# Kernel tuning notes

Measured on AMD Instinct MI355X. Metric: run time of the kernel, lower is better.

## Reference

```python
import jax, jax.numpy as jnp
import numpy as np

ALPHA = 0.9  # EMAFusion temporal_fusion_alpha


def setup_inputs() -> dict:
    key = jax.random.key(0)
    y_seq = jax.random.normal(key, (4, 4096, 2048), dtype=jnp.float32)
    return {"y_seq": y_seq}


def reference(y_seq):
    # EMA recurrence: h_t = (1-alpha)*y_t + alpha*h_{t-1}, h_{-1}=0.
    # Original torch code detaches h_prev each step (backward-only effect),
    # mirrored here with stop_gradient on the carry.
    B, S, D = y_seq.shape
    h0 = jnp.zeros((B, D), dtype=y_seq.dtype)

    def step(h_prev, y_t):
        h_prev = jax.lax.stop_gradient(h_prev)
        h_t = (1.0 - ALPHA) * y_t + ALPHA * h_prev
        return h_t, h_t

    # scan over time axis: move S to leading dim
    _, out = jax.lax.scan(step, h0, jnp.swapaxes(y_seq, 0, 1))  # (S, B, D)
    return jnp.swapaxes(out, 0, 1)  # (B, S, D)
```

## Files before the change

kernel.cpp:

```cpp
#include <hip/hip_runtime.h>


typedef float v4 __attribute__((ext_vector_type(4)));

constexpr int B  = 4;
constexpr int S  = 4096;
constexpr int D  = 2048;
constexpr int D4 = D / 4;
constexpr int L  = 128;
constexpr int W  = 64;

__global__ __launch_bounds__(256, 1) void ema_kernel(const v4* __restrict__ y,
                                                     v4* __restrict__ out) {
    const int d4 = blockIdx.x * blockDim.x + threadIdx.x;
    const int c  = blockIdx.y;
    const int b  = blockIdx.z;

    const long long base = (long long)b * S * D4 + d4;
    const int sm = c * L;

    v4 h = (v4)(0.0f);
    const v4* __restrict__ p;

    v4 b0, b1, b2, b3, b4, b5, b6, b7;

#define LOAD_ALL() do {            \
        b0 = p[0 * D4];            \
        b1 = p[1 * D4];            \
        b2 = p[2 * D4];            \
        b3 = p[3 * D4];            \
        b4 = p[4 * D4];            \
        b5 = p[5 * D4];            \
        b6 = p[6 * D4];            \
        b7 = p[7 * D4];            \
        p += 8 * D4;               \
    } while (0)

#define EMA(bi) h = 0.9f * h + 0.1f * (bi)

    if (c != 0) {
        p = y + base + (long long)(sm - W) * D4;
        LOAD_ALL();
        #pragma unroll 1
        for (int g = 0; g < W / 8 - 1; ++g) {
            EMA(b0); b0 = p[0 * D4];
            EMA(b1); b1 = p[1 * D4];
            EMA(b2); b2 = p[2 * D4];
            EMA(b3); b3 = p[3 * D4];
            EMA(b4); b4 = p[4 * D4];
            EMA(b5); b5 = p[5 * D4];
            EMA(b6); b6 = p[6 * D4];
            EMA(b7); b7 = p[7 * D4];
            p += 8 * D4;
        }
        EMA(b0); EMA(b1); EMA(b2); EMA(b3);
        EMA(b4); EMA(b5); EMA(b6); EMA(b7);
    } else {
        p = y + base;
    }

    v4* __restrict__ q = out + base + (long long)sm * D4;
    LOAD_ALL();

#define STEP(i, bi)                                         \
        EMA(bi);                                            \
        __builtin_nontemporal_store(h, q + (i) * D4);       \
        bi = p[(i) * D4]

    #pragma unroll 1
    for (int g = 0; g < L / 8 - 1; ++g) {
        STEP(0, b0);
        STEP(1, b1);
        STEP(2, b2);
        STEP(3, b3);
        STEP(4, b4);
        STEP(5, b5);
        STEP(6, b6);
        STEP(7, b7);
        p += 8 * D4;
        q += 8 * D4;
    }
    EMA(b0); __builtin_nontemporal_store(h, q + 0 * D4);
    EMA(b1); __builtin_nontemporal_store(h, q + 1 * D4);
    EMA(b2); __builtin_nontemporal_store(h, q + 2 * D4);
    EMA(b3); __builtin_nontemporal_store(h, q + 3 * D4);
    EMA(b4); __builtin_nontemporal_store(h, q + 4 * D4);
    EMA(b5); __builtin_nontemporal_store(h, q + 5 * D4);
    EMA(b6); __builtin_nontemporal_store(h, q + 6 * D4);
    EMA(b7); __builtin_nontemporal_store(h, q + 7 * D4);

#undef STEP
#undef EMA
#undef LOAD_ALL
}

extern "C" void kernel_launch(void* const* d_in, const int* in_sizes, int n_in,
                              void* d_out, int out_size, void* d_ws, size_t ws_size,
                              hipStream_t stream) {
    const v4* y = (const v4*)d_in[0];
    v4* out = (v4*)d_out;

    dim3 block(256, 1, 1);
    dim3 grid(D4 / 256, S / L, B);
    ema_kernel<<<grid, block, 0, stream>>>(y, out);
}
```

Baseline: 237.0 us.

## Shorten time chunks and raise occupancy with double-buffered EMA loads

Cuts the per-block time chunk from 128 to 32 steps and raises the launch bound to 4 blocks per CU, so four times as many blocks run and more loads are in flight. The load path now uses two 8-deep register buffers (a/b) so one batch is in flight while the other is consumed. Early chunks get a warmup window shortened to the available history instead of a special case. The trade-off is extra traffic: each block still replays a 64-step warmup for only 32 outputs, which triples the input reads compared with 1.5x before, though most of those rereads may hit cache.

```diff
diff --git a/kernel.cpp b/kernel.cpp
--- a/kernel.cpp
+++ b/kernel.cpp
@@ -7,10 +7,10 @@
 constexpr int S  = 4096;
 constexpr int D  = 2048;
 constexpr int D4 = D / 4;
-constexpr int L  = 128;
+constexpr int L  = 32;
 constexpr int W  = 64;
 
-__global__ __launch_bounds__(256, 1) void ema_kernel(const v4* __restrict__ y,
+__global__ __launch_bounds__(256, 4) void ema_kernel(const v4* __restrict__ y,
                                                      v4* __restrict__ out) {
     const int d4 = blockIdx.x * blockDim.x + threadIdx.x;
     const int c  = blockIdx.y;
@@ -22,9 +22,22 @@
     v4 h = (v4)(0.0f);
     const v4* __restrict__ p;
 
+    v4 a0, a1, a2, a3, a4, a5, a6, a7;
     v4 b0, b1, b2, b3, b4, b5, b6, b7;
 
-#define LOAD_ALL() do {            \
+#define LOADA() do {               \
+        a0 = p[0 * D4];            \
+        a1 = p[1 * D4];            \
+        a2 = p[2 * D4];            \
+        a3 = p[3 * D4];            \
+        a4 = p[4 * D4];            \
+        a5 = p[5 * D4];            \
+        a6 = p[6 * D4];            \
+        a7 = p[7 * D4];            \
+        p += 8 * D4;               \
+    } while (0)
+
+#define LOADB() do {               \
         b0 = p[0 * D4];            \
         b1 = p[1 * D4];            \
         b2 = p[2 * D4];            \
@@ -36,62 +49,75 @@
         p += 8 * D4;               \
     } while (0)
 
-#define EMA(bi) h = 0.9f * h + 0.1f * (bi)
+#define EMA(x) (h = 0.9f * h + 0.1f * (x))
+#define EMAA() do { EMA(a0); EMA(a1); EMA(a2); EMA(a3); \
+                    EMA(a4); EMA(a5); EMA(a6); EMA(a7); } while (0)
+#define EMAB() do { EMA(b0); EMA(b1); EMA(b2); EMA(b3); \
+                    EMA(b4); EMA(b5); EMA(b6); EMA(b7); } while (0)
 
-    if (c != 0) {
-        p = y + base + (long long)(sm - W) * D4;
-        LOAD_ALL();
+    const int nw = (sm < W) ? sm : W;
+    p = y + base + (long long)(sm - nw) * D4;
+
+    if (nw) {
+        LOADA();
+        LOADB();
         #pragma unroll 1
-        for (int g = 0; g < W / 8 - 1; ++g) {
-            EMA(b0); b0 = p[0 * D4];
-            EMA(b1); b1 = p[1 * D4];
-            EMA(b2); b2 = p[2 * D4];
-            EMA(b3); b3 = p[3 * D4];
-            EMA(b4); b4 = p[4 * D4];
-            EMA(b5); b5 = p[5 * D4];
-            EMA(b6); b6 = p[6 * D4];
-            EMA(b7); b7 = p[7 * D4];
-            p += 8 * D4;
+        for (int g = 0; g < (nw / 8 - 2) / 2; ++g) {
+            EMAA(); LOADA();
+            EMAB(); LOADB();
         }
-        EMA(b0); EMA(b1); EMA(b2); EMA(b3);
-        EMA(b4); EMA(b5); EMA(b6); EMA(b7);
-    } else {
-        p = y + base;
+        EMAA();
+        EMAB();
     }
 
     v4* __restrict__ q = out + base + (long long)sm * D4;
-    LOAD_ALL();
 
-#define STEP(i, bi)                                         \
-        EMA(bi);                                            \
-        __builtin_nontemporal_store(h, q + (i) * D4);       \
-        bi = p[(i) * D4]
+    LOADA();
+    LOADB();
 
-    #pragma unroll 1
-    for (int g = 0; g < L / 8 - 1; ++g) {
-        STEP(0, b0);
-        STEP(1, b1);
-        STEP(2, b2);
-        STEP(3, b3);
-        STEP(4, b4);
-        STEP(5, b5);
-        STEP(6, b6);
-        STEP(7, b7);
-        p += 8 * D4;
-        q += 8 * D4;
-    }
-    EMA(b0); __builtin_nontemporal_store(h, q + 0 * D4);
-    EMA(b1); __builtin_nontemporal_store(h, q + 1 * D4);
-    EMA(b2); __builtin_nontemporal_store(h, q + 2 * D4);
-    EMA(b3); __builtin_nontemporal_store(h, q + 3 * D4);
-    EMA(b4); __builtin_nontemporal_store(h, q + 4 * D4);
-    EMA(b5); __builtin_nontemporal_store(h, q + 5 * D4);
-    EMA(b6); __builtin_nontemporal_store(h, q + 6 * D4);
-    EMA(b7); __builtin_nontemporal_store(h, q + 7 * D4);
+    EMA(a0); __builtin_nontemporal_store(h, q + 0 * D4);
+    EMA(a1); __builtin_nontemporal_store(h, q + 1 * D4);
+    EMA(a2); __builtin_nontemporal_store(h, q + 2 * D4);
+    EMA(a3); __builtin_nontemporal_store(h, q + 3 * D4);
+    EMA(a4); __builtin_nontemporal_store(h, q + 4 * D4);
+    EMA(a5); __builtin_nontemporal_store(h, q + 5 * D4);
+    EMA(a6); __builtin_nontemporal_store(h, q + 6 * D4);
+    EMA(a7); __builtin_nontemporal_store(h, q + 7 * D4);
+    LOADA();
 
-#undef STEP
+    EMA(b0); __builtin_nontemporal_store(h, q +  8 * D4);
+    EMA(b1); __builtin_nontemporal_store(h, q +  9 * D4);
+    EMA(b2); __builtin_nontemporal_store(h, q + 10 * D4);
+    EMA(b3); __builtin_nontemporal_store(h, q + 11 * D4);
+    EMA(b4); __builtin_nontemporal_store(h, q + 12 * D4);
+    EMA(b5); __builtin_nontemporal_store(h, q + 13 * D4);
+    EMA(b6); __builtin_nontemporal_store(h, q + 14 * D4);
+    EMA(b7); __builtin_nontemporal_store(h, q + 15 * D4);
+    LOADB();
+
+    EMA(a0); __builtin_nontemporal_store(h, q + 16 * D4);
+    EMA(a1); __builtin_nontemporal_store(h, q + 17 * D4);
+    EMA(a2); __builtin_nontemporal_store(h, q + 18 * D4);
+    EMA(a3); __builtin_nontemporal_store(h, q + 19 * D4);
+    EMA(a4); __builtin_nontemporal_store(h, q + 20 * D4);
+    EMA(a5); __builtin_nontemporal_store(h, q + 21 * D4);
+    EMA(a6); __builtin_nontemporal_store(h, q + 22 * D4);
+    EMA(a7); __builtin_nontemporal_store(h, q + 23 * D4);
+
+    EMA(b0); __builtin_nontemporal_store(h, q + 24 * D4);
+    EMA(b1); __builtin_nontemporal_store(h, q + 25 * D4);
+    EMA(b2); __builtin_nontemporal_store(h, q + 26 * D4);
+    EMA(b3); __builtin_nontemporal_store(h, q + 27 * D4);
+    EMA(b4); __builtin_nontemporal_store(h, q + 28 * D4);
+    EMA(b5); __builtin_nontemporal_store(h, q + 29 * D4);
+    EMA(b6); __builtin_nontemporal_store(h, q + 30 * D4);
+    EMA(b7); __builtin_nontemporal_store(h, q + 31 * D4);
+
+#undef EMAB
+#undef EMAA
 #undef EMA
-#undef LOAD_ALL
+#undef LOADB
+#undef LOADA
 }
 
 extern "C" void kernel_launch(void* const* d_in, const int* in_sizes, int n_in,
```

Result: slower. 255.2 us (+7.7%).

## Stage EMA input through LDS with async global_load_lds double buffering

Applied to the files above, without the earlier changes.

Global loads of y now go directly into shared memory through the global-to-LDS load builtin, using two 8-step buffers per wave. Explicit vmcnt waits and scheduling barriers replace the compiler-scheduled register prefetch. The aim is to keep more loads in flight and free VGPRs, so the serial EMA chain is fed with fewer stalls. In exchange it adds LDS round trips and hand-placed waits. Because stores also count toward vmcnt on CDNA, the waits may end up stricter than the loads alone need.

```diff
diff --git a/kernel.cpp b/kernel.cpp
--- a/kernel.cpp
+++ b/kernel.cpp
@@ -8,90 +8,93 @@
 constexpr int D  = 2048;
 constexpr int D4 = D / 4;
 constexpr int L  = 128;
-constexpr int W  = 64;
+
+#define SEAL() __builtin_amdgcn_sched_barrier(0)
+#define WAIT8() do { asm volatile("s_waitcnt vmcnt(8)" ::: "memory"); SEAL(); } while (0)
+#define WAIT0() do { asm volatile("s_waitcnt vmcnt(0)" ::: "memory"); SEAL(); } while (0)
 
 __global__ __launch_bounds__(256, 1) void ema_kernel(const v4* __restrict__ y,
                                                      v4* __restrict__ out) {
-    const int d4 = blockIdx.x * blockDim.x + threadIdx.x;
-    const int c  = blockIdx.y;
-    const int b  = blockIdx.z;
+    __shared__ v4 smem[4096];
+
+    const int tid  = threadIdx.x;
+    const int wave = tid >> 6;
+    const int lane = tid & 63;
+    const int d4   = blockIdx.x * blockDim.x + tid;
+    const int c    = blockIdx.y;
+    const int b    = blockIdx.z;
 
     const long long base = (long long)b * S * D4 + d4;
-    const int sm = c * L;
+    const int sm  = c * L;
+    const int nwg = (c == 0) ? 0 : 8;
+
+    const v4* p = y + base + (long long)(sm - 8 * nwg) * D4;
+    v4* q = out + base + (long long)sm * D4;
 
     v4 h = (v4)(0.0f);
-    const v4* __restrict__ p;
 
-    v4 b0, b1, b2, b3, b4, b5, b6, b7;
+#define SLOT(kb, s) ((((kb) * 8 + (s)) * 4 + wave) * 64)
 
-#define LOAD_ALL() do {            \
-        b0 = p[0 * D4];            \
-        b1 = p[1 * D4];            \
-        b2 = p[2 * D4];            \
-        b3 = p[3 * D4];            \
-        b4 = p[4 * D4];            \
-        b5 = p[5 * D4];            \
-        b6 = p[6 * D4];            \
-        b7 = p[7 * D4];            \
-        p += 8 * D4;               \
+#define ISSUE1(kb, s) \
+    __builtin_amdgcn_global_load_lds(p + (s) * D4, &smem[SLOT(kb, s)], 16, 0, 0)
+
+#define ISSUE(kb) do {                                      \
+        ISSUE1(kb, 0); ISSUE1(kb, 1); ISSUE1(kb, 2); ISSUE1(kb, 3); \
+        ISSUE1(kb, 4); ISSUE1(kb, 5); ISSUE1(kb, 6); ISSUE1(kb, 7); \
+        p += 8 * D4;                                        \
+        SEAL();                                             \
     } while (0)
 
-#define EMA(bi) h = 0.9f * h + 0.1f * (bi)
+#define EMA1(kb, s) do {                                    \
+        v4 x = smem[SLOT(kb, s) + lane];                    \
+        h = 0.9f * h + 0.1f * x;                            \
+    } while (0)
+
+#define CONS_NS(kb) do {                                    \
+        EMA1(kb, 0); EMA1(kb, 1); EMA1(kb, 2); EMA1(kb, 3); \
+        EMA1(kb, 4); EMA1(kb, 5); EMA1(kb, 6); EMA1(kb, 7); \
+        SEAL();                                             \
+    } while (0)
+
+#define EMST1(kb, s) do {                                   \
+        v4 x = smem[SLOT(kb, s) + lane];                    \
+        h = 0.9f * h + 0.1f * x;                            \
+        __builtin_nontemporal_store(h, q + (s) * D4);       \
+    } while (0)
+
+#define CONS_ST(kb) do {                                    \
+        EMST1(kb, 0); EMST1(kb, 1); EMST1(kb, 2); EMST1(kb, 3); \
+        EMST1(kb, 4); EMST1(kb, 5); EMST1(kb, 6); EMST1(kb, 7); \
+        q += 8 * D4;                                        \
+        SEAL();                                             \
+    } while (0)
+
+    ISSUE(0);
+    ISSUE(1);
 
     if (c != 0) {
-        p = y + base + (long long)(sm - W) * D4;
-        LOAD_ALL();
         #pragma unroll 1
-        for (int g = 0; g < W / 8 - 1; ++g) {
-            EMA(b0); b0 = p[0 * D4];
-            EMA(b1); b1 = p[1 * D4];
-            EMA(b2); b2 = p[2 * D4];
-            EMA(b3); b3 = p[3 * D4];
-            EMA(b4); b4 = p[4 * D4];
-            EMA(b5); b5 = p[5 * D4];
-            EMA(b6); b6 = p[6 * D4];
-            EMA(b7); b7 = p[7 * D4];
-            p += 8 * D4;
+        for (int it = 0; it < 4; ++it) {
+            WAIT8(); CONS_NS(0); ISSUE(0);
+            WAIT8(); CONS_NS(1); ISSUE(1);
         }
-        EMA(b0); EMA(b1); EMA(b2); EMA(b3);
-        EMA(b4); EMA(b5); EMA(b6); EMA(b7);
-    } else {
-        p = y + base;
     }
 
-    v4* __restrict__ q = out + base + (long long)sm * D4;
-    LOAD_ALL();
+    #pragma unroll 1
+    for (int it = 0; it < 7; ++it) {
+        WAIT8(); CONS_ST(0); ISSUE(0);
+        WAIT8(); CONS_ST(1); ISSUE(1);
+    }
+    WAIT8(); CONS_ST(0);
+    WAIT0(); CONS_ST(1);
 
-#define STEP(i, bi)                                         \
-        EMA(bi);                                            \
-        __builtin_nontemporal_store(h, q + (i) * D4);       \
-        bi = p[(i) * D4]
-
-    #pragma unroll 1
-    for (int g = 0; g < L / 8 - 1; ++g) {
-        STEP(0, b0);
-        STEP(1, b1);
-        STEP(2, b2);
-        STEP(3, b3);
-        STEP(4, b4);
-        STEP(5, b5);
-        STEP(6, b6);
-        STEP(7, b7);
-        p += 8 * D4;
-        q += 8 * D4;
-    }
-    EMA(b0); __builtin_nontemporal_store(h, q + 0 * D4);
-    EMA(b1); __builtin_nontemporal_store(h, q + 1 * D4);
-    EMA(b2); __builtin_nontemporal_store(h, q + 2 * D4);
-    EMA(b3); __builtin_nontemporal_store(h, q + 3 * D4);
-    EMA(b4); __builtin_nontemporal_store(h, q + 4 * D4);
-    EMA(b5); __builtin_nontemporal_store(h, q + 5 * D4);
-    EMA(b6); __builtin_nontemporal_store(h, q + 6 * D4);
-    EMA(b7); __builtin_nontemporal_store(h, q + 7 * D4);
-
-#undef STEP
-#undef EMA
-#undef LOAD_ALL
+#undef CONS_ST
+#undef EMST1
+#undef CONS_NS
+#undef EMA1
+#undef ISSUE
+#undef ISSUE1
+#undef SLOT
 }
 
 extern "C" void kernel_launch(void* const* d_in, const int* in_sizes, int n_in,
```

Result: no change. 236.5 us (-0.2%).
